# Optimization experiments

Hardware: AMD Instinct MI355X
Metric: run time of the kernel (lower is better)

The kernel has to match this reference:

```python
import jax, jax.numpy as jnp
import numpy as np

N = 100000   # num nodes
E = 1000000  # num edges
IN = 64      # in_channels
H = 64       # hidden_dim
RESCUE_SCALE = 0.01


def setup_inputs() -> dict:
    key = jax.random.key(0)
    ks = jax.random.split(key, 8)
    x = jax.random.normal(ks[0], (N, IN), jnp.float32)
    edge_index = jax.random.randint(ks[1], (2, E), 0, N, dtype=jnp.int64)
    edge_weight = jax.random.uniform(ks[2], (E,), jnp.float32)
    glorot = lambda k, sh, fan: jax.random.normal(k, sh, jnp.float32) / np.sqrt(fan).astype(np.float32)
    W1 = glorot(ks[3], (IN, H), IN); b1 = jnp.zeros((H,), jnp.float32)
    W2 = glorot(ks[4], (H, H), H);  b2 = jnp.zeros((H,), jnp.float32)
    Wn = glorot(ks[5], (H, 1), H);  bn = jnp.zeros((1,), jnp.float32)
    Wr = glorot(ks[6], (H, 1), H);  br = jnp.zeros((1,), jnp.float32)
    return {"x": x, "edge_index": edge_index, "edge_weight": edge_weight,
            "W1": W1, "b1": b1, "W2": W2, "b2": b2,
            "Wn": Wn, "bn": bn, "Wr": Wr, "br": br}


def gcn_conv(x, src, dst, ew, W, b):
    # PyG GCNConv: linear first, then symmetric-normalized scatter-add aggregation.
    x = x @ W                                              # [N, H]
    deg = jax.ops.segment_sum(ew, dst, num_segments=N)     # weighted in-degree
    dinv = jnp.where(deg > 0, jax.lax.rsqrt(deg), 0.0)     # deg^{-1/2}, inf -> 0
    norm = dinv[src] * ew * dinv[dst]                      # [E+N]
    out = jax.ops.segment_sum(x[src] * norm[:, None], dst, num_segments=N)
    return out + b


def reference(x, edge_index, edge_weight, W1, b1, W2, b2, Wn, bn, Wr, br):
    # add self-loops with weight 1 (GCNConv default)
    loop = jnp.arange(N, dtype=edge_index.dtype)
    src = jnp.concatenate([edge_index[0], loop])
    dst = jnp.concatenate([edge_index[1], loop])
    ew = jnp.concatenate([edge_weight, jnp.ones((N,), edge_weight.dtype)])

    h = jax.nn.relu(gcn_conv(x, src, dst, ew, W1, b1))
    h = jax.nn.relu(gcn_conv(h, src, dst, ew, W2, b2))

    node_logits = (h @ Wn + bn).squeeze(-1)                # [N]
    node_selector = jax.nn.softmax(node_logits, axis=0)
    rescue_ratios = jax.nn.sigmoid((h @ Wr + br).squeeze(-1)) * RESCUE_SCALE
    return node_selector, rescue_ratios
```

## Files before the change

kernel.cpp:

```cpp
#include <hip/hip_runtime.h>
#include <hip/hip_fp16.h>
#include <math.h>

#define NN 100000
#define NE 1000000
#define CAP 32
#define OVCAP 4096
#define NEB 3907
#define NTILE 6250
#define RB 256

typedef _Float16 half8 __attribute__((ext_vector_type(8)));
typedef float f32x4 __attribute__((ext_vector_type(4)));


__global__ __launch_bounds__(256) void k_bucket(const int* __restrict__ src,
                                                const int* __restrict__ dst,
                                                const float* __restrict__ ew,
                                                int* __restrict__ cnt,
                                                int2* __restrict__ bucket,
                                                int4* __restrict__ ovf,
                                                int* __restrict__ ovf_n) {
  int e = blockIdx.x * 256 + threadIdx.x;
  if (e < NE) {
    int s = src[e];
    int d = dst[e];
    float w = ew[e];
    int pos = atomicAdd(&cnt[d], 1);
    if (pos < CAP) {
      bucket[d * CAP + pos] = make_int2(s, __float_as_int(w));
    } else {
      int t = atomicAdd(ovf_n, 1);
      if (t < OVCAP) ovf[t] = make_int4(s, d, __float_as_int(w), 0);
    }
  }
}


__device__ __forceinline__ void stage_B_lds(const float* __restrict__ W,
                                            _Float16* __restrict__ ldsB) {
  for (int u = threadIdx.x; u < 512; u += 256) {
    int slane = u & 63, ts = u >> 6;
    int t = ts >> 1, s = ts & 1;
    int qq = slane >> 4, ll = slane & 15;
#pragma unroll
    for (int j = 0; j < 8; ++j)
      ldsB[u * 8 + j] = (_Float16)W[(s * 32 + qq * 8 + j) * 64 + t * 16 + ll];
  }
}


__device__ __forceinline__ float degsum_row(const int* __restrict__ cnt,
                                            const int2* __restrict__ bucket,
                                            const int4* __restrict__ ovf,
                                            const int* __restrict__ ovf_n,
                                            int row) {
  int c = cnt[row];
  int cc = c < CAP ? c : CAP;
  float dsum = 1.0f;
  const int2* bk = bucket + (size_t)row * CAP;
  for (int j = 0; j < cc; ++j) dsum += __int_as_float(bk[j].y);
  if (c > CAP) {
    int on = ovf_n[0]; if (on > OVCAP) on = OVCAP;
    for (int t = 0; t < on; ++t) {
      int4 o = ovf[t];
      if (o.y == row) dsum += __int_as_float(o.z);
    }
  }
  return 1.0f / sqrtf(dsum);
}


__global__ __launch_bounds__(256) void k_gemm1_dinv(const float* __restrict__ X,
                                                    const float* __restrict__ W,
                                                    const int* __restrict__ cnt,
                                                    const int2* __restrict__ bucket,
                                                    const int4* __restrict__ ovf,
                                                    const int* __restrict__ ovf_n,
                                                    float* __restrict__ dinv,
                                                    __half* __restrict__ Y) {
  __shared__ _Float16 ldsB[4096];
  stage_B_lds(W, ldsB);
  __syncthreads();
  int lane = threadIdx.x & 63;
  int l15 = lane & 15, q = lane >> 4;
  half8 bfr[4][2];
#pragma unroll
  for (int t = 0; t < 4; ++t)
#pragma unroll
    for (int s = 0; s < 2; ++s)
      bfr[t][s] = *(half8*)&ldsB[((t * 2 + s) * 64 + lane) * 8];

  int wid = blockIdx.x * 4 + (threadIdx.x >> 6);
  for (int tile = wid; tile < NTILE; tile += 2048) {
    int row = tile * 16 + l15;
    float di = degsum_row(cnt, bucket, ovf, ovf_n, row);
    if (q == 0) dinv[row] = di;
    f32x4 acc[4] = {{0.f,0.f,0.f,0.f},{0.f,0.f,0.f,0.f},
                    {0.f,0.f,0.f,0.f},{0.f,0.f,0.f,0.f}};
#pragma unroll
    for (int s = 0; s < 2; ++s) {
      const float* ap = X + (size_t)row * 64 + s * 32 + q * 8;
      float4 a0 = *(const float4*)ap;
      float4 a1 = *(const float4*)(ap + 4);
      half8 af;
      af[0] = (_Float16)a0.x; af[1] = (_Float16)a0.y;
      af[2] = (_Float16)a0.z; af[3] = (_Float16)a0.w;
      af[4] = (_Float16)a1.x; af[5] = (_Float16)a1.y;
      af[6] = (_Float16)a1.z; af[7] = (_Float16)a1.w;
#pragma unroll
      for (int t = 0; t < 4; ++t)
        acc[t] = __builtin_amdgcn_mfma_f32_16x16x32_f16(af, bfr[t][s], acc[t], 0, 0, 0);
    }
#pragma unroll
    for (int r = 0; r < 4; ++r) {
      int rw = tile * 16 + q * 4 + r;
      float dv = __shfl(di, q * 4 + r, 64);
#pragma unroll
      for (int t = 0; t < 4; ++t)
        Y[(size_t)rw * 64 + t * 16 + l15] = __float2half(acc[t][r] * dv);
    }
  }
}


__device__ __forceinline__ float4 h4load(const __half* p) {
  float2 raw = *(const float2*)p;
  __half2 a = *(__half2*)&raw.x;
  __half2 b = *(__half2*)&raw.y;
  float2 fa = __half22float2(a), fb = __half22float2(b);
  return make_float4(fa.x, fa.y, fb.x, fb.y);
}

__device__ __forceinline__ float4 gather_node(const __half* __restrict__ xw,
                                              const int* __restrict__ cnt,
                                              const int2* __restrict__ bucket,
                                              const int4* __restrict__ ovf,
                                              const int* __restrict__ ovf_n,
                                              int node, int l) {
  int c = cnt[node];
  int cc = c < CAP ? c : CAP;
  const int4* bk4 = (const int4*)(bucket + (size_t)node * CAP);
  float4 acc = make_float4(0.f, 0.f, 0.f, 0.f);

  int j = 0;
  for (; j + 4 <= cc; j += 4) {
    int4 pa = bk4[j >> 1];
    int4 pb = bk4[(j >> 1) + 1];
    const float4 x0 = h4load(xw + (size_t)pa.x * 64 + l * 4);
    const float4 x1 = h4load(xw + (size_t)pa.z * 64 + l * 4);
    const float4 x2 = h4load(xw + (size_t)pb.x * 64 + l * 4);
    const float4 x3 = h4load(xw + (size_t)pb.z * 64 + l * 4);
    float v0 = __int_as_float(pa.y);
    float v1 = __int_as_float(pa.w);
    float v2 = __int_as_float(pb.y);
    float v3 = __int_as_float(pb.w);
    acc.x = fmaf(x0.x, v0, acc.x); acc.y = fmaf(x0.y, v0, acc.y);
    acc.z = fmaf(x0.z, v0, acc.z); acc.w = fmaf(x0.w, v0, acc.w);
    acc.x = fmaf(x1.x, v1, acc.x); acc.y = fmaf(x1.y, v1, acc.y);
    acc.z = fmaf(x1.z, v1, acc.z); acc.w = fmaf(x1.w, v1, acc.w);
    acc.x = fmaf(x2.x, v2, acc.x); acc.y = fmaf(x2.y, v2, acc.y);
    acc.z = fmaf(x2.z, v2, acc.z); acc.w = fmaf(x2.w, v2, acc.w);
    acc.x = fmaf(x3.x, v3, acc.x); acc.y = fmaf(x3.y, v3, acc.y);
    acc.z = fmaf(x3.z, v3, acc.z); acc.w = fmaf(x3.w, v3, acc.w);
  }
  const int2* bk = (const int2*)bk4;
  for (; j < cc; ++j) {
    int2 E = bk[j];
    const float4 xa = h4load(xw + (size_t)E.x * 64 + l * 4);
    float v = __int_as_float(E.y);
    acc.x = fmaf(xa.x, v, acc.x); acc.y = fmaf(xa.y, v, acc.y);
    acc.z = fmaf(xa.z, v, acc.z); acc.w = fmaf(xa.w, v, acc.w);
  }
  if (c > CAP) {
    int on = ovf_n[0]; if (on > OVCAP) on = OVCAP;
    for (int t = 0; t < on; ++t) {
      int4 o = ovf[t];
      if (o.y == node) {
        const float4 xa = h4load(xw + (size_t)o.x * 64 + l * 4);
        float v = __int_as_float(o.z);
        acc.x = fmaf(xa.x, v, acc.x); acc.y = fmaf(xa.y, v, acc.y);
        acc.z = fmaf(xa.z, v, acc.z); acc.w = fmaf(xa.w, v, acc.w);
      }
    }
  }
  const float4 xs = h4load(xw + (size_t)node * 64 + l * 4);
  acc.x += xs.x; acc.y += xs.y; acc.z += xs.z; acc.w += xs.w;
  return acc;
}


__global__ __launch_bounds__(256) void k_gather_gemm2(const __half* __restrict__ xw,
                                                      const float* __restrict__ dinv,
                                                      const int* __restrict__ cnt,
                                                      const int2* __restrict__ bucket,
                                                      const int4* __restrict__ ovf,
                                                      const int* __restrict__ ovf_n,
                                                      const float* __restrict__ b1,
                                                      const float* __restrict__ W2,
                                                      __half* __restrict__ Y) {
  __shared__ _Float16 ldsB[4096];
  __shared__ _Float16 ldsR[16 * 72];
  __shared__ float sdi[16];
  stage_B_lds(W2, ldsB);

  int l = threadIdx.x & 15;
  int g = threadIdx.x >> 4;
  int node = blockIdx.x * 16 + g;
  float4 acc = gather_node(xw, cnt, bucket, ovf, ovf_n, node, l);
  float di = dinv[node];
  const float4 b4 = *(const float4*)(b1 + l * 4);
  _Float16* rp = &ldsR[g * 72 + l * 4];
  rp[0] = (_Float16)fmaxf(fmaf(acc.x, di, b4.x), 0.f);
  rp[1] = (_Float16)fmaxf(fmaf(acc.y, di, b4.y), 0.f);
  rp[2] = (_Float16)fmaxf(fmaf(acc.z, di, b4.z), 0.f);
  rp[3] = (_Float16)fmaxf(fmaf(acc.w, di, b4.w), 0.f);
  if (l == 0) sdi[g] = di;
  __syncthreads();

  int lane = threadIdx.x & 63;
  int l15 = lane & 15, q = lane >> 4;
  int t = threadIdx.x >> 6;
  half8 a0 = *(half8*)&ldsR[l15 * 72 + q * 8];
  half8 a1 = *(half8*)&ldsR[l15 * 72 + 32 + q * 8];
  half8 bf0 = *(half8*)&ldsB[((t * 2 + 0) * 64 + lane) * 8];
  half8 bf1 = *(half8*)&ldsB[((t * 2 + 1) * 64 + lane) * 8];
  f32x4 acc2 = {0.f, 0.f, 0.f, 0.f};
  acc2 = __builtin_amdgcn_mfma_f32_16x16x32_f16(a0, bf0, acc2, 0, 0, 0);
  acc2 = __builtin_amdgcn_mfma_f32_16x16x32_f16(a1, bf1, acc2, 0, 0, 0);
#pragma unroll
  for (int r = 0; r < 4; ++r) {
    int rw = blockIdx.x * 16 + q * 4 + r;
    float dv = sdi[q * 4 + r];
    Y[(size_t)rw * 64 + t * 16 + l15] = __float2half(acc2[r] * dv);
  }
}


__global__ __launch_bounds__(256) void k_gather_l2_heads(const __half* __restrict__ xw2,
                                                         const float* __restrict__ dinv,
                                                         const int* __restrict__ cnt,
                                                         const int2* __restrict__ bucket,
                                                         const int4* __restrict__ ovf,
                                                         const int* __restrict__ ovf_n,
                                                         const float* __restrict__ b2,
                                                         const float* __restrict__ Wn,
                                                         const float* __restrict__ bn,
                                                         const float* __restrict__ Wr,
                                                         const float* __restrict__ br,
                                                         float* __restrict__ logits,
                                                         float* __restrict__ rr,
                                                         float* __restrict__ part) {
  __shared__ float s[256];
  int l = threadIdx.x & 15;
  int node = blockIdx.x * 16 + (threadIdx.x >> 4);
  float4 acc = gather_node(xw2, cnt, bucket, ovf, ovf_n, node, l);
  float di = dinv[node];
  const float4 b4 = *(const float4*)(b2 + l * 4);
  float4 r;
  r.x = fmaxf(fmaf(acc.x, di, b4.x), 0.f); r.y = fmaxf(fmaf(acc.y, di, b4.y), 0.f);
  r.z = fmaxf(fmaf(acc.z, di, b4.z), 0.f); r.w = fmaxf(fmaf(acc.w, di, b4.w), 0.f);
  const float4 wn4 = *(const float4*)(Wn + l * 4);
  const float4 wr4 = *(const float4*)(Wr + l * 4);
  float an = r.x * wn4.x + r.y * wn4.y + r.z * wn4.z + r.w * wn4.w;
  float ar = r.x * wr4.x + r.y * wr4.y + r.z * wr4.z + r.w * wr4.w;
#pragma unroll
  for (int m = 8; m > 0; m >>= 1) {
    an += __shfl_xor(an, m, 64);
    ar += __shfl_xor(ar, m, 64);
  }
  float lg = an + bn[0];
  if (l == 0) {
    logits[node] = lg;
    float xr = ar + br[0];
    rr[node] = 0.01f / (1.0f + expf(-xr));
  }
  s[threadIdx.x] = lg;
  __syncthreads();
  for (int w = 128; w > 0; w >>= 1) {
    if (threadIdx.x < w) s[threadIdx.x] = fmaxf(s[threadIdx.x], s[threadIdx.x + w]);
    __syncthreads();
  }
  if (threadIdx.x == 0) part[blockIdx.x] = s[0];
}


__global__ __launch_bounds__(256) void k_sexp(const float* __restrict__ logits,
                                              const float* __restrict__ part,
                                              float* __restrict__ sel,
                                              float* __restrict__ gsum) {
  __shared__ float s[256];
  float m = -INFINITY;
  for (int i = threadIdx.x; i < NTILE; i += 256) m = fmaxf(m, part[i]);
  s[threadIdx.x] = m;
  __syncthreads();
  for (int w = 128; w > 0; w >>= 1) {
    if (threadIdx.x < w) s[threadIdx.x] = fmaxf(s[threadIdx.x], s[threadIdx.x + w]);
    __syncthreads();
  }
  float gm = s[0];
  __syncthreads();
  float acc = 0.0f;
  for (int i = blockIdx.x * 256 + threadIdx.x; i < NN; i += RB * 256) {
    float e = expf(logits[i] - gm);
    sel[i] = e;
    acc += e;
  }
  s[threadIdx.x] = acc;
  __syncthreads();
  for (int w = 128; w > 0; w >>= 1) {
    if (threadIdx.x < w) s[threadIdx.x] += s[threadIdx.x + w];
    __syncthreads();
  }
  if (threadIdx.x == 0) unsafeAtomicAdd(gsum, s[0]);
}

__global__ __launch_bounds__(256) void k_snorm(float* __restrict__ sel,
                                               const float* __restrict__ gsum) {
  int i = blockIdx.x * 256 + threadIdx.x;
  if (i < NN) sel[i] *= (1.0f / gsum[0]);
}


extern "C" void kernel_launch(void* const* d_in, const int* in_sizes, int n_in,
                              void* d_out, int out_size, void* d_ws, size_t ws_size,
                              hipStream_t stream) {
  const float* x  = (const float*)d_in[0];
  const int*   ei = (const int*)d_in[1];
  const float* ew = (const float*)d_in[2];
  const float* W1 = (const float*)d_in[3];
  const float* b1 = (const float*)d_in[4];
  const float* W2 = (const float*)d_in[5];
  const float* b2 = (const float*)d_in[6];
  const float* Wn = (const float*)d_in[7];
  const float* bn = (const float*)d_in[8];
  const float* Wr = (const float*)d_in[9];
  const float* br = (const float*)d_in[10];
  const int* src = ei;
  const int* dst = ei + NE;

  char* wsb = (char*)d_ws;
  __half* xw     = (__half*)wsb;
  __half* xw2    = (__half*)(wsb + 12800000);
  float*  dinv   = (float*)(wsb + 25600000);
  float*  logits = (float*)(wsb + 26000000);
  int2*   bucket = (int2*)(wsb + 26400000);
  int4*   ovf    = (int4*)(wsb + 52000000);
  int*    cnt    = (int*)(wsb + 52065536);
  int*    ovf_n  = cnt + NN;
  float*  gsum   = (float*)(ovf_n + 1);
  float*  part1  = gsum + 1;

  float* sel = (float*)d_out;
  float* rr  = (float*)d_out + NN;

  int gN = (NN + 255) / 256;

  hipMemsetAsync(cnt, 0, (size_t)(NN + 2) * 4, stream);

  k_bucket<<<NEB, 256, 0, stream>>>(src, dst, ew, cnt, bucket, ovf, ovf_n);

  k_gemm1_dinv<<<512, 256, 0, stream>>>(x, W1, cnt, bucket, ovf, ovf_n, dinv, xw);

  k_gather_gemm2<<<NTILE, 256, 0, stream>>>(xw, dinv, cnt, bucket, ovf, ovf_n,
                                            b1, W2, xw2);

  k_gather_l2_heads<<<NTILE, 256, 0, stream>>>(xw2, dinv, cnt, bucket, ovf, ovf_n,
                                               b2, Wn, bn, Wr, br, logits, rr, part1);

  k_sexp<<<RB, 256, 0, stream>>>(logits, part1, sel, gsum);
  k_snorm<<<gN, 256, 0, stream>>>(sel, gsum);
}
```

Before: 250.7 us.

## Fuse edge bucketing with layer-1 GEMM and accumulate degree via atomics

```diff
diff --git a/kernel.cpp b/kernel.cpp
--- a/kernel.cpp
+++ b/kernel.cpp
@@ -9,32 +9,10 @@
 #define NEB 3907
 #define NTILE 6250
 #define RB 256
+#define GB1 512
 
 typedef _Float16 half8 __attribute__((ext_vector_type(8)));
 typedef float f32x4 __attribute__((ext_vector_type(4)));
-
-
-__global__ __launch_bounds__(256) void k_bucket(const int* __restrict__ src,
-                                                const int* __restrict__ dst,
-                                                const float* __restrict__ ew,
-                                                int* __restrict__ cnt,
-                                                int2* __restrict__ bucket,
-                                                int4* __restrict__ ovf,
-                                                int* __restrict__ ovf_n) {
-  int e = blockIdx.x * 256 + threadIdx.x;
-  if (e < NE) {
-    int s = src[e];
-    int d = dst[e];
-    float w = ew[e];
-    int pos = atomicAdd(&cnt[d], 1);
-    if (pos < CAP) {
-      bucket[d * CAP + pos] = make_int2(s, __float_as_int(w));
-    } else {
-      int t = atomicAdd(ovf_n, 1);
-      if (t < OVCAP) ovf[t] = make_int4(s, d, __float_as_int(w), 0);
-    }
-  }
-}
 
 
 __device__ __forceinline__ void stage_B_lds(const float* __restrict__ W,
@@ -50,37 +28,36 @@
 }
 
 
-__device__ __forceinline__ float degsum_row(const int* __restrict__ cnt,
-                                            const int2* __restrict__ bucket,
-                                            const int4* __restrict__ ovf,
-                                            const int* __restrict__ ovf_n,
-                                            int row) {
-  int c = cnt[row];
-  int cc = c < CAP ? c : CAP;
-  float dsum = 1.0f;
-  const int2* bk = bucket + (size_t)row * CAP;
-  for (int j = 0; j < cc; ++j) dsum += __int_as_float(bk[j].y);
-  if (c > CAP) {
-    int on = ovf_n[0]; if (on > OVCAP) on = OVCAP;
-    for (int t = 0; t < on; ++t) {
-      int4 o = ovf[t];
-      if (o.y == row) dsum += __int_as_float(o.z);
-    }
-  }
-  return 1.0f / sqrtf(dsum);
-}
-
-
-__global__ __launch_bounds__(256) void k_gemm1_dinv(const float* __restrict__ X,
-                                                    const float* __restrict__ W,
-                                                    const int* __restrict__ cnt,
-                                                    const int2* __restrict__ bucket,
-                                                    const int4* __restrict__ ovf,
-                                                    const int* __restrict__ ovf_n,
-                                                    float* __restrict__ dinv,
-                                                    __half* __restrict__ Y) {
+__global__ __launch_bounds__(256) void k_bucket_gemm1(const int* __restrict__ src,
+                                                      const int* __restrict__ dst,
+                                                      const float* __restrict__ ew,
+                                                      const float* __restrict__ X,
+                                                      const float* __restrict__ W1,
+                                                      int* __restrict__ cnt,
+                                                      float* __restrict__ deg,
+                                                      int2* __restrict__ bucket,
+                                                      int4* __restrict__ ovf,
+                                                      int* __restrict__ ovf_n,
+                                                      __half* __restrict__ Y) {
   __shared__ _Float16 ldsB[4096];
-  stage_B_lds(W, ldsB);
+  if (blockIdx.x >= GB1) {
+    int e = (blockIdx.x - GB1) * 256 + threadIdx.x;
+    if (e < NE) {
+      int s = src[e];
+      int d = dst[e];
+      float w = ew[e];
+      int pos = atomicAdd(&cnt[d], 1);
+      unsafeAtomicAdd(&deg[d], w);
+      if (pos < CAP) {
+        bucket[d * CAP + pos] = make_int2(s, __float_as_int(w));
+      } else {
+        int t = atomicAdd(ovf_n, 1);
+        if (t < OVCAP) ovf[t] = make_int4(s, d, __float_as_int(w), 0);
+      }
+    }
+    return;
+  }
+  stage_B_lds(W1, ldsB);
   __syncthreads();
   int lane = threadIdx.x & 63;
   int l15 = lane & 15, q = lane >> 4;
@@ -92,10 +69,8 @@
       bfr[t][s] = *(half8*)&ldsB[((t * 2 + s) * 64 + lane) * 8];
 
   int wid = blockIdx.x * 4 + (threadIdx.x >> 6);
-  for (int tile = wid; tile < NTILE; tile += 2048) {
+  for (int tile = wid; tile < NTILE; tile += GB1 * 4) {
     int row = tile * 16 + l15;
-    float di = degsum_row(cnt, bucket, ovf, ovf_n, row);
-    if (q == 0) dinv[row] = di;
     f32x4 acc[4] = {{0.f,0.f,0.f,0.f},{0.f,0.f,0.f,0.f},
                     {0.f,0.f,0.f,0.f},{0.f,0.f,0.f,0.f}};
 #pragma unroll
@@ -115,12 +90,17 @@
 #pragma unroll
     for (int r = 0; r < 4; ++r) {
       int rw = tile * 16 + q * 4 + r;
-      float dv = __shfl(di, q * 4 + r, 64);
 #pragma unroll
       for (int t = 0; t < 4; ++t)
-        Y[(size_t)rw * 64 + t * 16 + l15] = __float2half(acc[t][r] * dv);
-    }
-  }
+        Y[(size_t)rw * 64 + t * 16 + l15] = __float2half(acc[t][r]);
+    }
+  }
+}
+
+
+__global__ __launch_bounds__(256) void k_dinv(float* __restrict__ deg) {
+  int i = blockIdx.x * 256 + threadIdx.x;
+  if (i < NN) deg[i] = 1.0f / sqrtf(deg[i] + 1.0f);
 }
 
 
@@ -132,12 +112,14 @@
   return make_float4(fa.x, fa.y, fb.x, fb.y);
 }
 
+template <bool FOLD>
 __device__ __forceinline__ float4 gather_node(const __half* __restrict__ xw,
                                               const int* __restrict__ cnt,
                                               const int2* __restrict__ bucket,
                                               const int4* __restrict__ ovf,
                                               const int* __restrict__ ovf_n,
-                                              int node, int l) {
+                                              const float* __restrict__ dinv,
+                                              int node, int l, float selfw) {
   int c = cnt[node];
   int cc = c < CAP ? c : CAP;
   const int4* bk4 = (const int4*)(bucket + (size_t)node * CAP);
@@ -155,6 +137,10 @@
     float v1 = __int_as_float(pa.w);
     float v2 = __int_as_float(pb.y);
     float v3 = __int_as_float(pb.w);
+    if (FOLD) {
+      v0 *= dinv[pa.x]; v1 *= dinv[pa.z];
+      v2 *= dinv[pb.x]; v3 *= dinv[pb.z];
+    }
     acc.x = fmaf(x0.x, v0, acc.x); acc.y = fmaf(x0.y, v0, acc.y);
     acc.z = fmaf(x0.z, v0, acc.z); acc.w = fmaf(x0.w, v0, acc.w);
     acc.x = fmaf(x1.x, v1, acc.x); acc.y = fmaf(x1.y, v1, acc.y);
@@ -169,6 +155,7 @@
     int2 E = bk[j];
     const float4 xa = h4load(xw + (size_t)E.x * 64 + l * 4);
     float v = __int_as_float(E.y);
+    if (FOLD) v *= dinv[E.x];
     acc.x = fmaf(xa.x, v, acc.x); acc.y = fmaf(xa.y, v, acc.y);
     acc.z = fmaf(xa.z, v, acc.z); acc.w = fmaf(xa.w, v, acc.w);
   }
@@ -179,13 +166,15 @@
       if (o.y == node) {
         const float4 xa = h4load(xw + (size_t)o.x * 64 + l * 4);
         float v = __int_as_float(o.z);
+        if (FOLD) v *= dinv[o.x];
         acc.x = fmaf(xa.x, v, acc.x); acc.y = fmaf(xa.y, v, acc.y);
         acc.z = fmaf(xa.z, v, acc.z); acc.w = fmaf(xa.w, v, acc.w);
       }
     }
   }
   const float4 xs = h4load(xw + (size_t)node * 64 + l * 4);
-  acc.x += xs.x; acc.y += xs.y; acc.z += xs.z; acc.w += xs.w;
+  acc.x = fmaf(xs.x, selfw, acc.x); acc.y = fmaf(xs.y, selfw, acc.y);
+  acc.z = fmaf(xs.z, selfw, acc.z); acc.w = fmaf(xs.w, selfw, acc.w);
   return acc;
 }
 
@@ -207,8 +196,8 @@
   int l = threadIdx.x & 15;
   int g = threadIdx.x >> 4;
   int node = blockIdx.x * 16 + g;
-  float4 acc = gather_node(xw, cnt, bucket, ovf, ovf_n, node, l);
   float di = dinv[node];
+  float4 acc = gather_node<true>(xw, cnt, bucket, ovf, ovf_n, dinv, node, l, di);
   const float4 b4 = *(const float4*)(b1 + l * 4);
   _Float16* rp = &ldsR[g * 72 + l * 4];
   rp[0] = (_Float16)fmaxf(fmaf(acc.x, di, b4.x), 0.f);
@@ -254,7 +243,7 @@
   __shared__ float s[256];
   int l = threadIdx.x & 15;
   int node = blockIdx.x * 16 + (threadIdx.x >> 4);
-  float4 acc = gather_node(xw2, cnt, bucket, ovf, ovf_n, node, l);
+  float4 acc = gather_node<false>(xw2, cnt, bucket, ovf, ovf_n, dinv, node, l, 1.0f);
   float di = dinv[node];
   const float4 b4 = *(const float4*)(b2 + l * 4);
   float4 r;
@@ -342,30 +331,31 @@
   char* wsb = (char*)d_ws;
   __half* xw     = (__half*)wsb;
   __half* xw2    = (__half*)(wsb + 12800000);
-  float*  dinv   = (float*)(wsb + 25600000);
-  float*  logits = (float*)(wsb + 26000000);
-  int2*   bucket = (int2*)(wsb + 26400000);
-  int4*   ovf    = (int4*)(wsb + 52000000);
-  int*    cnt    = (int*)(wsb + 52065536);
-  int*    ovf_n  = cnt + NN;
-  float*  gsum   = (float*)(ovf_n + 1);
-  float*  part1  = gsum + 1;
+  float*  logits = (float*)(wsb + 25600000);
+  int2*   bucket = (int2*)(wsb + 26000000);
+  int4*   ovf    = (int4*)(wsb + 51600000);
+  int*    cnt    = (int*)(wsb + 51665536);
+  float*  deg    = (float*)(wsb + 52065536);
+  int*    ovf_n  = (int*)(wsb + 52465536);
+  float*  gsum   = (float*)(wsb + 52465540);
+  float*  part1  = (float*)(wsb + 52465544);
 
   float* sel = (float*)d_out;
   float* rr  = (float*)d_out + NN;
 
   int gN = (NN + 255) / 256;
 
-  hipMemsetAsync(cnt, 0, (size_t)(NN + 2) * 4, stream);
-
-  k_bucket<<<NEB, 256, 0, stream>>>(src, dst, ew, cnt, bucket, ovf, ovf_n);
-
-  k_gemm1_dinv<<<512, 256, 0, stream>>>(x, W1, cnt, bucket, ovf, ovf_n, dinv, xw);
-
-  k_gather_gemm2<<<NTILE, 256, 0, stream>>>(xw, dinv, cnt, bucket, ovf, ovf_n,
+  hipMemsetAsync(cnt, 0, (size_t)(2 * NN + 2) * 4, stream);
+
+  k_bucket_gemm1<<<GB1 + NEB, 256, 0, stream>>>(src, dst, ew, x, W1,
+                                                cnt, deg, bucket, ovf, ovf_n, xw);
+
+  k_dinv<<<gN, 256, 0, stream>>>(deg);
+
+  k_gather_gemm2<<<NTILE, 256, 0, stream>>>(xw, deg, cnt, bucket, ovf, ovf_n,
                                             b1, W2, xw2);
 
-  k_gather_l2_heads<<<NTILE, 256, 0, stream>>>(xw2, dinv, cnt, bucket, ovf, ovf_n,
+  k_gather_l2_heads<<<NTILE, 256, 0, stream>>>(xw2, deg, cnt, bucket, ovf, ovf_n,
                                                b2, Wn, bn, Wr, br, logits, rr, part1);
 
   k_sexp<<<RB, 256, 0, stream>>>(logits, part1, sel, gsum);
```

New measurement: 264.5 us. 1.06x slower.
